# Kernel tuning notes

Measured on AMD Instinct MI355X. Metric: run time of the kernel, lower is better.

Reference implementation:

```python
import jax, jax.numpy as jnp
import numpy as np
from math import pi as PI, log

B, N, D, K = 16, 16384, 64, 64


def setup_inputs() -> dict:
    key = jax.random.key(0)
    k1, k2, k3, k4 = jax.random.split(key, 4)
    x = jax.random.normal(k1, (B, N, D), dtype=jnp.float32)
    pi_w = jax.nn.softmax(jax.random.normal(k2, (K,), dtype=jnp.float32))  # mixture weights, sum to 1
    mu = jax.random.normal(k3, (K, D), dtype=jnp.float32)
    var = jax.random.uniform(k4, (K, D), dtype=jnp.float32, minval=0.5, maxval=1.5)  # diagonal variances
    return {"x": x, "pi": pi_w, "mu": mu, "var": var}


def reference(x, pi, mu, var):
    b, n, d = x.shape
    # --- gmm.predict_proba: diagonal-covariance Gaussian log-likelihoods + log pi, softmax over K ---
    inv_var = 1.0 / var                                   # (K, D)
    x2 = x * x                                            # (B, N, D)
    # Mahalanobis distance expanded via matmuls to avoid a (B,N,K,D) intermediate
    maha = (jnp.einsum('bnd,kd->bnk', x2, inv_var)
            - 2.0 * jnp.einsum('bnd,kd->bnk', x, mu * inv_var)
            + jnp.sum(mu * mu * inv_var, axis=-1))        # (B, N, K)
    log_det = jnp.sum(jnp.log(var), axis=-1)              # (K,)
    log_prob = -0.5 * (d * log(2.0 * PI) + log_det + maha)
    Q = jax.nn.softmax(log_prob + jnp.log(pi), axis=-1)   # (B, N, K) responsibilities
    # --- weighted reductions over N ---
    Q_sum = jnp.sum(Q, axis=1) / n                         # (B, K)
    Q_x = jnp.einsum('bnk,bnd->bkd', Q, x) / n             # (B, K, D)
    Q_x2 = jnp.einsum('bnk,bnd->bkd', Q, x2) / n           # (B, K, D)
    # --- Fisher-vector statistics ---
    d_pi = Q_sum - pi                                      # (B, K)
    qs = Q_sum[..., None]                                  # (B, K, 1)
    d_mu = Q_x - qs * mu
    d_sigma = -Q_x2 - qs * (mu * mu) + qs * var + 2.0 * Q_x * mu
    return jnp.concatenate([d_pi.reshape(b, -1), d_mu.reshape(b, -1), d_sigma.reshape(b, -1)], axis=1)
```

## Files before the change

### kernel.cpp

```cpp
#include <hip/hip_runtime.h>
#include <hip/hip_bf16.h>
#include <math.h>

#define B_  16
#define N_  16384
#define D_  64
#define K_  64
#define OUT_PER_B (K_ + 2*K_*D_)
#define CHUNKS 64
#define NTILES (N_ / CHUNKS / 64)

#define PART_STRIDE (64*4 + 2*4096*2)

typedef float f32x4 __attribute__((ext_vector_type(4)));
typedef short short8 __attribute__((ext_vector_type(8)));

union U8 { short8 s8; unsigned int u[4]; };

__device__ __forceinline__ unsigned short f2bf(float f) {
    union { float f; unsigned int u; } v; v.f = f;
    unsigned int r = v.u + 0x7FFFu + ((v.u >> 16) & 1u);
    return (unsigned short)(r >> 16);
}

__device__ __forceinline__ unsigned int f2bf2(float lo, float hi) {
    __hip_bfloat162 h = __float22bfloat162_rn(make_float2(lo, hi));
    unsigned int u;
    __builtin_memcpy(&u, &h, 4);
    return u;
}

__device__ __forceinline__ float bf2f(unsigned short u) {
    unsigned int v = ((unsigned int)u) << 16;
    float f;
    __builtin_memcpy(&f, &v, 4);
    return f;
}

__global__ __launch_bounds__(256, 2) void fv_main(const float* __restrict__ x,
                                                  const float* __restrict__ pi,
                                                  const float* __restrict__ mu,
                                                  const float* __restrict__ var,
                                                  char* __restrict__ partials) {
    __shared__ __align__(16) unsigned short QtS[2][64 * 72];
    __shared__ float qsum_s[4][64];
    __shared__ float red[256];
    __shared__ float c0s[64];

    const int t    = threadIdx.x;
    const int w    = t >> 6;
    const int lane = t & 63;
    const int r16  = lane & 15;
    const int q    = lane >> 4;

    {
        int k = t >> 2, pr = t & 3;
        float s = 0.0f;
        #pragma unroll
        for (int j = 0; j < 16; ++j) {
            int d = pr * 16 + j;
            float v = var[k * 64 + d];
            float m = mu[k * 64 + d];
            s += __logf(v) + m * m / v;
        }
        red[t] = s;
    }

    short8 wfrag[4][4];
    #pragma unroll
    for (int kt = 0; kt < 4; ++kt) {
        const int k = 16 * kt + r16;
        const float* vr = var + k * 64 + 8 * q;
        const float* mr = mu  + k * 64 + 8 * q;
        float vv[16], mm[16];
        *(float4*)&vv[0]  = *(const float4*)(vr);
        *(float4*)&vv[4]  = *(const float4*)(vr + 4);
        *(float4*)&vv[8]  = *(const float4*)(vr + 32);
        *(float4*)&vv[12] = *(const float4*)(vr + 36);
        *(float4*)&mm[0]  = *(const float4*)(mr);
        *(float4*)&mm[4]  = *(const float4*)(mr + 4);
        *(float4*)&mm[8]  = *(const float4*)(mr + 32);
        *(float4*)&mm[12] = *(const float4*)(mr + 36);
        float iv[16];
        #pragma unroll
        for (int i = 0; i < 16; ++i) iv[i] = 1.0f / vv[i];
        U8 h0, h1, h2, h3;
        #pragma unroll
        for (int i = 0; i < 4; ++i) {
            h0.u[i] = f2bf2(-0.5f * iv[2*i],     -0.5f * iv[2*i + 1]);
            h1.u[i] = f2bf2(-0.5f * iv[8 + 2*i], -0.5f * iv[8 + 2*i + 1]);
            h2.u[i] = f2bf2(mm[2*i] * iv[2*i],   mm[2*i+1] * iv[2*i + 1]);
            h3.u[i] = f2bf2(mm[8+2*i] * iv[8+2*i], mm[8+2*i+1] * iv[8+2*i+1]);
        }
        wfrag[kt][0] = h0.s8; wfrag[kt][1] = h1.s8;
        wfrag[kt][2] = h2.s8; wfrag[kt][3] = h3.s8;
    }

    __syncthreads();
    if ((t & 3) == 0) {
        int k = t >> 2;
        float sum = red[4 * k] + red[4 * k + 1] + red[4 * k + 2] + red[4 * k + 3];
        c0s[k] = __logf(pi[k]) - 0.5f * (117.6241322502f + sum);
    }
    __syncthreads();

    f32x4 c0v[4];
    #pragma unroll
    for (int kt = 0; kt < 4; ++kt)
        c0v[kt] = *(const f32x4*)&c0s[16 * kt + 4 * q];

    const int bi    = blockIdx.y;
    const int chunk = blockIdx.x;
    const int ppb   = N_ / CHUNKS;
    const float* xb = x + ((size_t)bi * N_ + (size_t)chunk * ppb) * D_;

    f32x4 accX[4]  = {};
    f32x4 accX2[4] = {};
    float qsacc[4][4] = {};

    const int rowoff = (16 * w + r16) * D_ + 8 * q;
    const int dcol   = 16 * w + r16;

    float4 va, vb, vc, vd;
    {
        const float* xr = xb + rowoff;
        va = *(const float4*)(xr);
        vb = *(const float4*)(xr + 4);
        vc = *(const float4*)(xr + 32);
        vd = *(const float4*)(xr + 36);
    }

    #pragma unroll 2
    for (int tile = 0; tile < NTILES; ++tile) {
        const float* xt = xb + (size_t)tile * 64 * D_;

        float vle[16];
        {
            const float* xc = xt + dcol;
            #pragma unroll
            for (int c = 0; c < 2; ++c)
                #pragma unroll
                for (int j = 0; j < 8; ++j)
                    vle[8 * c + j] = xc[(32 * c + 8 * q + j) * D_];
        }

        float4 nva, nvb, nvc, nvd;
        if (tile + 1 < NTILES) {
            const float* xr = xt + 64 * D_ + rowoff;
            nva = *(const float4*)(xr);
            nvb = *(const float4*)(xr + 4);
            nvc = *(const float4*)(xr + 32);
            nvd = *(const float4*)(xr + 36);
        }

        U8 fxa, fxb, fx2a, fx2b;
        fxa.u[0]  = f2bf2(va.x, va.y);           fxa.u[1]  = f2bf2(va.z, va.w);
        fxa.u[2]  = f2bf2(vb.x, vb.y);           fxa.u[3]  = f2bf2(vb.z, vb.w);
        fxb.u[0]  = f2bf2(vc.x, vc.y);           fxb.u[1]  = f2bf2(vc.z, vc.w);
        fxb.u[2]  = f2bf2(vd.x, vd.y);           fxb.u[3]  = f2bf2(vd.z, vd.w);
        fx2a.u[0] = f2bf2(va.x*va.x, va.y*va.y); fx2a.u[1] = f2bf2(va.z*va.z, va.w*va.w);
        fx2a.u[2] = f2bf2(vb.x*vb.x, vb.y*vb.y); fx2a.u[3] = f2bf2(vb.z*vb.z, vb.w*vb.w);
        fx2b.u[0] = f2bf2(vc.x*vc.x, vc.y*vc.y); fx2b.u[1] = f2bf2(vc.z*vc.z, vc.w*vc.w);
        fx2b.u[2] = f2bf2(vd.x*vd.x, vd.y*vd.y); fx2b.u[3] = f2bf2(vd.z*vd.z, vd.w*vd.w);

        float sc[4][4];
        #pragma unroll
        for (int kt = 0; kt < 4; ++kt) {
            f32x4 a = c0v[kt];
            a = __builtin_amdgcn_mfma_f32_16x16x32_bf16(wfrag[kt][0], fx2a.s8, a, 0, 0, 0);
            a = __builtin_amdgcn_mfma_f32_16x16x32_bf16(wfrag[kt][1], fx2b.s8, a, 0, 0, 0);
            a = __builtin_amdgcn_mfma_f32_16x16x32_bf16(wfrag[kt][2], fxa.s8,  a, 0, 0, 0);
            a = __builtin_amdgcn_mfma_f32_16x16x32_bf16(wfrag[kt][3], fxb.s8,  a, 0, 0, 0);
            sc[kt][0] = a[0]; sc[kt][1] = a[1]; sc[kt][2] = a[2]; sc[kt][3] = a[3];
        }

        float mx = sc[0][0];
        #pragma unroll
        for (int kt = 0; kt < 4; ++kt)
            #pragma unroll
            for (int rr = 0; rr < 4; ++rr) mx = fmaxf(mx, sc[kt][rr]);
        mx = fmaxf(mx, __shfl_xor(mx, 16));
        mx = fmaxf(mx, __shfl_xor(mx, 32));
        float z = 0.0f;
        #pragma unroll
        for (int kt = 0; kt < 4; ++kt)
            #pragma unroll
            for (int rr = 0; rr < 4; ++rr) {
                sc[kt][rr] = __expf(sc[kt][rr] - mx);
                z += sc[kt][rr];
            }
        z += __shfl_xor(z, 16);
        z += __shfl_xor(z, 32);
        float inv = 1.0f / z;
        const int p = 16 * w + r16;
        unsigned short* Qb = QtS[tile & 1];
        #pragma unroll
        for (int kt = 0; kt < 4; ++kt) {
            #pragma unroll
            for (int rr = 0; rr < 4; rr += 2) {
                float q0 = sc[kt][rr] * inv;
                float q1 = sc[kt][rr + 1] * inv;
                qsacc[kt][rr]     += q0;
                qsacc[kt][rr + 1] += q1;
                unsigned int pk = f2bf2(q0, q1);
                Qb[(16 * kt + 4 * q + rr)     * 72 + p] = (unsigned short)pk;
                Qb[(16 * kt + 4 * q + rr + 1) * 72 + p] = (unsigned short)(pk >> 16);
            }
        }

        asm volatile("s_waitcnt lgkmcnt(0)\n\ts_barrier" ::: "memory");

        U8 fxp0, fxp1, fx2p0, fx2p1;
        #pragma unroll
        for (int i = 0; i < 4; ++i) {
            float a0 = vle[2 * i], a1 = vle[2 * i + 1];
            float b0 = vle[8 + 2 * i], b1 = vle[8 + 2 * i + 1];
            fxp0.u[i]  = f2bf2(a0, a1);
            fxp1.u[i]  = f2bf2(b0, b1);
            fx2p0.u[i] = f2bf2(a0 * a0, a1 * a1);
            fx2p1.u[i] = f2bf2(b0 * b0, b1 * b1);
        }
        #pragma unroll
        for (int kt = 0; kt < 4; ++kt) {
            const unsigned short* qr = &Qb[(16 * kt + r16) * 72 + 8 * q];
            short8 aq0 = *(const short8*)(const void*)(qr);
            short8 aq1 = *(const short8*)(const void*)(qr + 32);
            accX[kt]  = __builtin_amdgcn_mfma_f32_16x16x32_bf16(aq0, fxp0.s8,  accX[kt],  0, 0, 0);
            accX2[kt] = __builtin_amdgcn_mfma_f32_16x16x32_bf16(aq0, fx2p0.s8, accX2[kt], 0, 0, 0);
            accX[kt]  = __builtin_amdgcn_mfma_f32_16x16x32_bf16(aq1, fxp1.s8,  accX[kt],  0, 0, 0);
            accX2[kt] = __builtin_amdgcn_mfma_f32_16x16x32_bf16(aq1, fx2p1.s8, accX2[kt], 0, 0, 0);
        }

        va = nva; vb = nvb; vc = nvc; vd = nvd;
    }

    char* rec = partials + ((size_t)bi * CHUNKS + chunk) * PART_STRIDE;
    float* part_qs = (float*)rec;
    unsigned short* part_qx  = (unsigned short*)(rec + 256);
    unsigned short* part_qx2 = part_qx + 4096;
    #pragma unroll
    for (int kt = 0; kt < 4; ++kt)
        #pragma unroll
        for (int rr = 0; rr < 4; ++rr) {
            int k = 16 * kt + 4 * q + rr;
            part_qx [k * 64 + 16 * w + r16] = f2bf(accX[kt][rr]);
            part_qx2[k * 64 + 16 * w + r16] = f2bf(accX2[kt][rr]);
        }
    #pragma unroll
    for (int kt = 0; kt < 4; ++kt)
        #pragma unroll
        for (int rr = 0; rr < 4; ++rr) {
            float v = qsacc[kt][rr];
            v += __shfl_xor(v, 1);
            v += __shfl_xor(v, 2);
            v += __shfl_xor(v, 4);
            v += __shfl_xor(v, 8);
            if (r16 == 0) qsum_s[w][16 * kt + 4 * q + rr] = v;
        }
    __syncthreads();
    if (t < 64)
        part_qs[t] = qsum_s[0][t] + qsum_s[1][t] + qsum_s[2][t] + qsum_s[3][t];
}

__global__ __launch_bounds__(256) void fv_finalize(const float* __restrict__ pi,
                                                   const float* __restrict__ mu,
                                                   const float* __restrict__ var,
                                                   const char* __restrict__ partials,
                                                   float* __restrict__ out) {
    const int bk = blockIdx.x;
    const int b  = bk >> 6;
    const int k  = bk & 63;
    const int t  = threadIdx.x;
    const int d  = t & 63;
    const int cg = t >> 6;

    const char* base = partials + (size_t)b * CHUNKS * PART_STRIDE;

    float qs = 0.0f, qx = 0.0f, qx2 = 0.0f;
    for (int c = cg; c < CHUNKS; c += 4) {
        const char* r = base + (size_t)c * PART_STRIDE;
        qs  += ((const float*)r)[k];
        qx  += bf2f(((const unsigned short*)(r + 256))[k * 64 + d]);
        qx2 += bf2f(((const unsigned short*)(r + 256))[4096 + k * 64 + d]);
    }

    __shared__ float sQx[4][64];
    __shared__ float sQx2[4][64];
    __shared__ float sQs[4];
    sQx[cg][d]  = qx;
    sQx2[cg][d] = qx2;
    if (d == 0) sQs[cg] = qs;
    __syncthreads();

    if (cg == 0) {
        const float invN = 1.0f / (float)N_;
        float QX  = sQx[0][d]  + sQx[1][d]  + sQx[2][d]  + sQx[3][d];
        float QX2 = sQx2[0][d] + sQx2[1][d] + sQx2[2][d] + sQx2[3][d];
        float QS  = sQs[0] + sQs[1] + sQs[2] + sQs[3];
        float m = mu[k * 64 + d];
        float v = var[k * 64 + d];
        float* ob = out + (size_t)b * OUT_PER_B;
        if (d == 0) ob[k] = QS * invN - pi[k];
        ob[64 + k * 64 + d]        = (QX - QS * m) * invN;
        ob[64 + 4096 + k * 64 + d] = (-QX2 - QS * m * m + QS * v + 2.0f * QX * m) * invN;
    }
}

extern "C" void kernel_launch(void* const* d_in, const int* in_sizes, int n_in,
                              void* d_out, int out_size, void* d_ws, size_t ws_size,
                              hipStream_t stream) {
    const float* x   = (const float*)d_in[0];
    const float* pi  = (const float*)d_in[1];
    const float* mu  = (const float*)d_in[2];
    const float* var = (const float*)d_in[3];
    char* partials = (char*)d_ws;

    fv_main<<<dim3(CHUNKS, B_), 256, 0, stream>>>(x, pi, mu, var, partials);
    fv_finalize<<<B_ * K_, 256, 0, stream>>>(pi, mu, var, partials, (float*)d_out);
}
```

Baseline: 134.9 us.

## Precompute GMM weight fragments in prep kernel and stage them via LDS

Moves the per-block computation of bf16 MFMA weight fragments and the per-component constants into a separate single-block prep kernel that writes them to workspace. The main kernel then loads the fragments into shared memory instead of holding 16 short8 registers, and raises launch bounds to 3 blocks per CU. This removes redundant parameter setup in every block and cuts register pressure to allow higher occupancy. The cost is an extra kernel launch, extra LDS traffic for the weights on every MFMA, and more LDS per block.

```diff
diff --git a/kernel.cpp b/kernel.cpp
--- a/kernel.cpp
+++ b/kernel.cpp
@@ -11,6 +11,9 @@
 #define NTILES (N_ / CHUNKS / 64)
 
 #define PART_STRIDE (64*4 + 2*4096*2)
+#define PART_TOTAL  ((size_t)B_ * CHUNKS * PART_STRIDE)
+#define W_OFF   PART_TOTAL
+#define C0_OFF  (PART_TOTAL + 16384)
 
 typedef float f32x4 __attribute__((ext_vector_type(4)));
 typedef short short8 __attribute__((ext_vector_type(8)));
@@ -37,21 +40,12 @@
     return f;
 }
 
-__global__ __launch_bounds__(256, 2) void fv_main(const float* __restrict__ x,
-                                                  const float* __restrict__ pi,
-                                                  const float* __restrict__ mu,
-                                                  const float* __restrict__ var,
-                                                  char* __restrict__ partials) {
-    __shared__ __align__(16) unsigned short QtS[2][64 * 72];
-    __shared__ float qsum_s[4][64];
+__global__ __launch_bounds__(256) void fv_prep(const float* __restrict__ pi,
+                                               const float* __restrict__ mu,
+                                               const float* __restrict__ var,
+                                               char* __restrict__ ws) {
     __shared__ float red[256];
-    __shared__ float c0s[64];
-
-    const int t    = threadIdx.x;
-    const int w    = t >> 6;
-    const int lane = t & 63;
-    const int r16  = lane & 15;
-    const int q    = lane >> 4;
+    const int t = threadIdx.x;
 
     {
         int k = t >> 2, pr = t & 3;
@@ -66,9 +60,11 @@
         red[t] = s;
     }
 
-    short8 wfrag[4][4];
-    #pragma unroll
-    for (int kt = 0; kt < 4; ++kt) {
+    {
+        const int lane = t & 63;
+        const int kt   = t >> 6;
+        const int r16  = lane & 15;
+        const int q    = lane >> 4;
         const int k = 16 * kt + r16;
         const float* vr = var + k * 64 + 8 * q;
         const float* mr = mu  + k * 64 + 8 * q;
@@ -92,22 +88,46 @@
             h2.u[i] = f2bf2(mm[2*i] * iv[2*i],   mm[2*i+1] * iv[2*i + 1]);
             h3.u[i] = f2bf2(mm[8+2*i] * iv[8+2*i], mm[8+2*i+1] * iv[8+2*i+1]);
         }
-        wfrag[kt][0] = h0.s8; wfrag[kt][1] = h1.s8;
-        wfrag[kt][2] = h2.s8; wfrag[kt][3] = h3.s8;
+        short8* W = (short8*)(ws + W_OFF);
+        W[(kt * 4 + 0) * 64 + lane] = h0.s8;
+        W[(kt * 4 + 1) * 64 + lane] = h1.s8;
+        W[(kt * 4 + 2) * 64 + lane] = h2.s8;
+        W[(kt * 4 + 3) * 64 + lane] = h3.s8;
     }
 
     __syncthreads();
     if ((t & 3) == 0) {
         int k = t >> 2;
         float sum = red[4 * k] + red[4 * k + 1] + red[4 * k + 2] + red[4 * k + 3];
-        c0s[k] = __logf(pi[k]) - 0.5f * (117.6241322502f + sum);
-    }
-    __syncthreads();
-
+        ((float*)(ws + C0_OFF))[k] = __logf(pi[k]) - 0.5f * (117.6241322502f + sum);
+    }
+}
+
+__global__ __launch_bounds__(256, 3) void fv_main(const float* __restrict__ x,
+                                                  char* __restrict__ partials) {
+    __shared__ __align__(16) unsigned short QtS[2][64 * 72];
+    __shared__ __align__(16) unsigned short wfS[4 * 4 * 64 * 8];
+    __shared__ float qsum_s[4][64];
+
+    const int t    = threadIdx.x;
+    const int w    = t >> 6;
+    const int lane = t & 63;
+    const int r16  = lane & 15;
+    const int q    = lane >> 4;
+
+    {
+        const float4* gw = (const float4*)(partials + W_OFF);
+        float4* sw = (float4*)wfS;
+        #pragma unroll
+        for (int i = 0; i < 4; ++i) sw[i * 256 + t] = gw[i * 256 + t];
+    }
     f32x4 c0v[4];
-    #pragma unroll
-    for (int kt = 0; kt < 4; ++kt)
-        c0v[kt] = *(const f32x4*)&c0s[16 * kt + 4 * q];
+    {
+        const float* c0g = (const float*)(partials + C0_OFF);
+        #pragma unroll
+        for (int kt = 0; kt < 4; ++kt)
+            c0v[kt] = *(const f32x4*)&c0g[16 * kt + 4 * q];
+    }
 
     const int bi    = blockIdx.y;
     const int chunk = blockIdx.x;
@@ -129,6 +149,10 @@
         vc = *(const float4*)(xr + 32);
         vd = *(const float4*)(xr + 36);
     }
+
+    const short8* wfp = (const short8*)wfS;
+
+    __syncthreads();
 
     #pragma unroll 2
     for (int tile = 0; tile < NTILES; ++tile) {
@@ -167,10 +191,10 @@
         #pragma unroll
         for (int kt = 0; kt < 4; ++kt) {
             f32x4 a = c0v[kt];
-            a = __builtin_amdgcn_mfma_f32_16x16x32_bf16(wfrag[kt][0], fx2a.s8, a, 0, 0, 0);
-            a = __builtin_amdgcn_mfma_f32_16x16x32_bf16(wfrag[kt][1], fx2b.s8, a, 0, 0, 0);
-            a = __builtin_amdgcn_mfma_f32_16x16x32_bf16(wfrag[kt][2], fxa.s8,  a, 0, 0, 0);
-            a = __builtin_amdgcn_mfma_f32_16x16x32_bf16(wfrag[kt][3], fxb.s8,  a, 0, 0, 0);
+            a = __builtin_amdgcn_mfma_f32_16x16x32_bf16(wfp[(kt*4+0)*64 + lane], fx2a.s8, a, 0, 0, 0);
+            a = __builtin_amdgcn_mfma_f32_16x16x32_bf16(wfp[(kt*4+1)*64 + lane], fx2b.s8, a, 0, 0, 0);
+            a = __builtin_amdgcn_mfma_f32_16x16x32_bf16(wfp[(kt*4+2)*64 + lane], fxa.s8,  a, 0, 0, 0);
+            a = __builtin_amdgcn_mfma_f32_16x16x32_bf16(wfp[(kt*4+3)*64 + lane], fxb.s8,  a, 0, 0, 0);
             sc[kt][0] = a[0]; sc[kt][1] = a[1]; sc[kt][2] = a[2]; sc[kt][3] = a[3];
         }
 
@@ -313,8 +337,9 @@
     const float* pi  = (const float*)d_in[1];
     const float* mu  = (const float*)d_in[2];
     const float* var = (const float*)d_in[3];
-    char* partials = (char*)d_ws;
-
-    fv_main<<<dim3(CHUNKS, B_), 256, 0, stream>>>(x, pi, mu, var, partials);
-    fv_finalize<<<B_ * K_, 256, 0, stream>>>(pi, mu, var, partials, (float*)d_out);
-}
+    char* ws = (char*)d_ws;
+
+    fv_prep<<<1, 256, 0, stream>>>(pi, mu, var, ws);
+    fv_main<<<dim3(CHUNKS, B_), 256, 0, stream>>>(x, ws);
+    fv_finalize<<<B_ * K_, 256, 0, stream>>>(pi, mu, var, ws, (float*)d_out);
+}
```

Result: faster. 122.4 us (-9.2%).
